# Kernel optimization log

Hardware: AMD Instinct MI355X
Metric: run time of the kernel (lower is better)

## Reference

```python
import jax, jax.numpy as jnp
import numpy as np

B, D, H, C = 8192, 2048, 4096, 64
HALF = D // 2
BLOCKS = 2


def setup_inputs() -> dict:
    key = jax.random.key(0)
    ks = jax.random.split(key, 8)
    z = jax.random.normal(ks[0], (B, D), jnp.float32)
    condition = jax.random.normal(ks[1], (B, C), jnp.float32)
    # alternating masks: block 0 identity=odd indices, transform=even; block 1 flipped
    even = jnp.arange(0, D, 2, dtype=jnp.int32)
    odd = jnp.arange(1, D, 2, dtype=jnp.int32)
    idx_id = jnp.stack([odd, even])   # [BLOCKS, HALF]
    idx_tr = jnp.stack([even, odd])   # [BLOCKS, HALF]
    def init_w(k, shape, fan_in):
        return jax.random.normal(k, shape, jnp.float32) * np.float32(1.0 / np.sqrt(fan_in))
    W1 = init_w(ks[2], (BLOCKS, HALF + C, H), HALF + C)
    b1 = jnp.zeros((BLOCKS, H), jnp.float32)
    W2 = init_w(ks[3], (BLOCKS, H, H), H)
    b2 = jnp.zeros((BLOCKS, H), jnp.float32)
    W3 = init_w(ks[4], (BLOCKS, H, 2 * HALF), H) * np.float32(0.01)  # keep exp(S) tame
    b3 = jnp.zeros((BLOCKS, 2 * HALF), jnp.float32)
    return {"z": z, "condition": condition, "idx_id": idx_id, "idx_tr": idx_tr,
            "W1": W1, "b1": b1, "W2": W2, "b2": b2, "W3": W3, "b3": b3}


def reference(z, condition, idx_id, idx_tr, W1, b1, W2, b2, W3, b3):
    # F_zx of the affine coupling layer (scale_tanh=False, clamp_scale=None)
    x = z
    log_det = jnp.zeros((z.shape[0], 1), z.dtype)
    for i in range(BLOCKS):
        # gather identity channels, condition on external vector
        h = jnp.concatenate([x[:, idx_id[i]], condition], axis=-1)  # [B, HALF+C]
        h = jax.nn.relu(h @ W1[i] + b1[i])
        h = jax.nn.relu(h @ W2[i] + b2[i])
        out = (h @ W3[i] + b3[i]).reshape(x.shape[0], HALF, 2)
        S = out[..., 0]  # scale logits
        T = out[..., 1]  # translation
        # scatter-update transformed channels
        x = x.at[:, idx_tr[i]].set(x[:, idx_tr[i]] * jnp.exp(S) + T)
        log_det = log_det + jnp.sum(S, axis=1, keepdims=True)
    return x, log_det
```

## Files before the change

### kernel.cpp

```cpp
#include <hip/hip_runtime.h>
#include <hip/hip_bf16.h>

#define B_    8192
#define D_    2048
#define H_    4096
#define C_    64
#define HALF_ 1024
#define KIN_  1088

typedef __attribute__((ext_vector_type(8))) short bf16x8;
typedef __attribute__((ext_vector_type(4))) float f32x4;

__device__ __forceinline__ unsigned short f2bf(float f) {
  __hip_bfloat16 h = __float2bfloat16(f);
  return *reinterpret_cast<unsigned short*>(&h);
}

__device__ __forceinline__ void gload16(const void* g, void* s) {
  __builtin_amdgcn_global_load_lds((const __attribute__((address_space(1))) void*)g,
                                   (__attribute__((address_space(3))) void*)s,
                                   16, 0, 0);
}

__global__ void convT(const float* __restrict__ W, unsigned short* __restrict__ Wt,
                      int K, int N) {
  __shared__ float tile[32][33];
  int tx = threadIdx.x & 31, ty = threadIdx.x >> 5;
  int n0 = blockIdx.x * 32, k0 = blockIdx.y * 32;
#pragma unroll
  for (int i = 0; i < 4; ++i)
    tile[ty + i * 8][tx] = W[(size_t)(k0 + ty + i * 8) * N + n0 + tx];
  __syncthreads();
#pragma unroll
  for (int i = 0; i < 4; ++i)
    Wt[(size_t)(n0 + ty + i * 8) * K + k0 + tx] = f2bf(tile[tx][ty + i * 8]);
}

__global__ void build_act(const float* __restrict__ xsrc, const float* __restrict__ cond,
                          int par, unsigned short* __restrict__ A0) {
  int row = blockIdx.y;
  int col = blockIdx.x * 256 + threadIdx.x;
  if (col >= KIN_) return;
  float v;
  if (col < HALF_) {
    float2 p = ((const float2*)xsrc)[(size_t)row * (D_ / 2) + col];
    v = par ? p.y : p.x;
  } else {
    v = cond[(size_t)row * C_ + (col - HALF_)];
  }
  A0[(size_t)row * KIN_ + col] = f2bf(v);
}

template <int MODE>
__global__ __launch_bounds__(512, 2)
void gemm8p(const unsigned short* __restrict__ A,
            const unsigned short* __restrict__ Bt,
            const float* __restrict__ bias,
            unsigned short* __restrict__ Cout,
            const float* __restrict__ xold, float* __restrict__ xnew,
            float* __restrict__ part, int par,
            int M, int N, int K) {
  __shared__ unsigned short lds[65536];
  char* ldsb = (char*)lds;
  const int tid = threadIdx.x;
  const int w = tid >> 6, lane = tid & 63;
  const int fr = lane & 15, fq = lane >> 4;
  const int wr = w >> 2, wc = w & 3;

  const int nbx = N >> 8;
  const int nwg = (int)gridDim.x;
  const int cpx = nwg >> 3;
  const int bid = (int)blockIdx.x;
  const int swz = (bid & 7) * cpx + (bid >> 3);
  const int by = swz / nbx, bx = swz - by * nbx;
  const int m0 = by << 8, n0 = bx << 8;

  const int chunkp = (((fr & 1) << 2) | fq) ^ (fr >> 1);
  const int A0 = (wr * 64 + (fr >> 1)) * 128 + chunkp * 16;
  const int B0 = 16384 + (wc * 32 + (fr >> 1)) * 128 + chunkp * 16;

  int rS[2], kcolS[2];
#pragma unroll
  for (int s = 0; s < 2; ++s) {
    int q = s * 512 + w * 64 + lane;
    int p = q >> 3, cph = q & 7;
    int clg = cph ^ (p & 7);
    rS[s] = 2 * p + (clg >> 2);
    kcolS[s] = (clg & 3) * 8;
  }
  const unsigned short* sA0 = A + (size_t)(m0 + rS[0]) * K + kcolS[0];
  const unsigned short* sA1 = A + (size_t)(m0 + rS[1]) * K + kcolS[1];
  const unsigned short* sB0 = Bt + (size_t)(n0 + rS[0]) * K + kcolS[0];
  const unsigned short* sB1 = Bt + (size_t)(n0 + rS[1]) * K + kcolS[1];
  const int dst0 = w * 1024 + lane * 16;

#define STAGE_ALL(OFF) do {                                                  \
    gload16(sA0, ldsb + (OFF) + dst0);                                       \
    gload16(sA1, ldsb + (OFF) + 8192 + dst0);                                \
    gload16(sB0, ldsb + (OFF) + 16384 + dst0);                               \
    gload16(sB1, ldsb + (OFF) + 24576 + dst0);                               \
    sA0 += 32; sA1 += 32; sB0 += 32; sB1 += 32;                              \
  } while (0)

#define RDFRAGS(AV, BV, OFF)                                                 \
    _Pragma("unroll") for (int n = 0; n < 4; ++n)                            \
      BV[n] = *(const bf16x8*)(ldsb + (OFF) + B0 + n * 1024);                \
    _Pragma("unroll") for (int m = 0; m < 8; ++m)                            \
      AV[m] = *(const bf16x8*)(ldsb + (OFF) + A0 + m * 1024);

#define MFMA32(AV, BV)                                                       \
    __builtin_amdgcn_s_setprio(1);                                           \
    _Pragma("unroll") for (int m = 0; m < 8; ++m)                            \
      _Pragma("unroll") for (int n = 0; n < 4; ++n)                          \
        acc[m][n] = __builtin_amdgcn_mfma_f32_16x16x32_bf16(                 \
            AV[m], BV[n], acc[m][n], 0, 0, 0);                               \
    __builtin_amdgcn_s_setprio(0);

#define WIN(STG, VM, RD, AVr, BVr, AVm, BVm)                                 \
  {                                                                          \
    if (STG) STAGE_ALL(stg);                                                 \
    if (VM == 1) asm volatile("s_waitcnt vmcnt(4)" ::: "memory");            \
    if (VM == 2) asm volatile("s_waitcnt vmcnt(0)" ::: "memory");            \
    __builtin_amdgcn_sched_barrier(0);                                       \
    __builtin_amdgcn_s_barrier();                                            \
    if (RD) { RDFRAGS(AVr, BVr, nxt) }                                       \
    MFMA32(AVm, BVm)                                                         \
    int _t = cur; cur = nxt; nxt = stg; stg = _t;                            \
  }

  f32x4 acc[8][4];
  f32x4 z4 = {0.f, 0.f, 0.f, 0.f};
#pragma unroll
  for (int m = 0; m < 8; ++m)
#pragma unroll
    for (int n = 0; n < 4; ++n) acc[m][n] = z4;

  const int NT = K >> 5;

  bf16x8 av0[8], bv0[4], av1[8], bv1[4];

  STAGE_ALL(0);
  STAGE_ALL(32768);
  asm volatile("s_waitcnt vmcnt(4)" ::: "memory");
  __builtin_amdgcn_sched_barrier(0);
  __builtin_amdgcn_s_barrier();
  RDFRAGS(av0, bv0, 0)
  int cur = 0, nxt = 32768, stg = 65536;

  for (int P = 0; P < (NT - 2) / 2; ++P) {
    WIN(1, 1, 1, av1, bv1, av0, bv0)
    WIN(1, 1, 1, av0, bv0, av1, bv1)
  }
  WIN(0, 2, 1, av1, bv1, av0, bv0)
  WIN(0, 0, 0, av1, bv1, av1, bv1)
  __builtin_amdgcn_s_barrier();
#undef WIN
#undef MFMA32
#undef RDFRAGS
#undef STAGE_ALL

  if (MODE == 0) {
#pragma unroll
    for (int m = 0; m < 8; ++m)
#pragma unroll
      for (int n = 0; n < 4; ++n) {
        int gcol = n0 + wc * 64 + n * 16 + fr;
        float bb = bias[gcol];
#pragma unroll
        for (int r = 0; r < 4; ++r) {
          float v = fmaxf(acc[m][n][r] + bb, 0.f);
          int lrow = m * 16 + fq * 4 + r;
          *(unsigned short*)(ldsb + w * 16384 + lrow * 128 + ((n ^ fq) * 32) + fr * 2) = f2bf(v);
        }
      }
    asm volatile("s_waitcnt lgkmcnt(0)" ::: "memory");
    __builtin_amdgcn_sched_barrier(0);
    unsigned short* Cb = Cout + (size_t)(m0 + wr * 128) * N + n0 + wc * 64;
    const int sub = lane & 7;
#pragma unroll
    for (int i = 0; i < 16; ++i) {
      int lrow = i * 8 + (lane >> 3);
      int phys = (sub >> 1) ^ ((lrow >> 2) & 3);
      bf16x8 val = *(const bf16x8*)(ldsb + w * 16384 + lrow * 128 + phys * 32 + (sub & 1) * 16);
      *(bf16x8*)(Cb + (size_t)lrow * N + sub * 8) = val;
    }
  } else {
#pragma unroll
    for (int m = 0; m < 8; ++m) {
      float srow[4] = {0.f, 0.f, 0.f, 0.f};
#pragma unroll
      for (int n = 0; n < 4; ++n) {
        int gcol = n0 + wc * 64 + n * 16 + fr;
        float bb = bias[gcol];
#pragma unroll
        for (int r = 0; r < 4; ++r) {
          float v = acc[m][n][r] + bb;
          float vp = __shfl_xor(v, 1);
          if (!(fr & 1)) {
            int grow = m0 + wr * 128 + m * 16 + fq * 4 + r;
            size_t idx = (size_t)grow * N + gcol + par;
            xnew[idx] = xold[idx] * expf(v) + vp;
            srow[r] += v;
          }
        }
      }
#pragma unroll
      for (int r = 0; r < 4; ++r) {
        float s = srow[r];
        s += __shfl_xor(s, 2);
        s += __shfl_xor(s, 4);
        s += __shfl_xor(s, 8);
        if (fr == 0) {
          int grow = m0 + wr * 128 + m * 16 + fq * 4 + r;
          part[(size_t)grow * 32 + bx * 4 + wc] = s;
        }
      }
    }
  }
}

__global__ void reduce_logdet(const float* __restrict__ P, float* __restrict__ logdet, int add) {
  int row = blockIdx.x * 256 + threadIdx.x;
  float s = 0.f;
#pragma unroll
  for (int g = 0; g < 32; ++g) s += P[(size_t)row * 32 + g];
  logdet[row] = add ? (logdet[row] + s) : s;
}

extern "C" void kernel_launch(void* const* d_in, const int* in_sizes, int n_in,
                              void* d_out, int out_size, void* d_ws, size_t ws_size,
                              hipStream_t stream) {
  const float* z    = (const float*)d_in[0];
  const float* cond = (const float*)d_in[1];
  const float* W1   = (const float*)d_in[4];
  const float* b1   = (const float*)d_in[5];
  const float* W2   = (const float*)d_in[6];
  const float* b2   = (const float*)d_in[7];
  const float* W3   = (const float*)d_in[8];
  const float* b3   = (const float*)d_in[9];

  float* xout   = (float*)d_out;
  float* logdet = xout + (size_t)B_ * D_;

  char* ws = (char*)d_ws;
  unsigned short* Wt = (unsigned short*)ws;
  unsigned short* H1 = (unsigned short*)(ws + 33554432);
  unsigned short* H2 = (unsigned short*)(ws + 33554432 + 67108864);
  float* Pp = (float*)H1;
  unsigned short* A0 = H2;

  for (int blk = 0; blk < 2; ++blk) {
    const float* W1b = W1 + (size_t)blk * KIN_ * H_;
    const float* W2b = W2 + (size_t)blk * H_ * H_;
    const float* W3b = W3 + (size_t)blk * H_ * D_;
    const float* b1b = b1 + (size_t)blk * H_;
    const float* b2b = b2 + (size_t)blk * H_;
    const float* b3b = b3 + (size_t)blk * D_;
    const float* xsrc = blk ? xout : z;

    convT<<<dim3(H_ / 32, KIN_ / 32), 256, 0, stream>>>(W1b, Wt, KIN_, H_);
    build_act<<<dim3(5, B_), 256, 0, stream>>>(xsrc, cond, 1 - blk, A0);
    gemm8p<0><<<dim3((H_ / 256) * (B_ / 256)), 512, 0, stream>>>(
        A0, Wt, b1b, H1, nullptr, nullptr, nullptr, 0, B_, H_, KIN_);

    convT<<<dim3(H_ / 32, H_ / 32), 256, 0, stream>>>(W2b, Wt, H_, H_);
    gemm8p<0><<<dim3((H_ / 256) * (B_ / 256)), 512, 0, stream>>>(
        H1, Wt, b2b, H2, nullptr, nullptr, nullptr, 0, B_, H_, H_);

    convT<<<dim3(D_ / 32, H_ / 32), 256, 0, stream>>>(W3b, Wt, H_, D_);
    gemm8p<1><<<dim3((D_ / 256) * (B_ / 256)), 512, 0, stream>>>(
        H2, Wt, b3b, nullptr, z, xout, Pp, blk, B_, D_, H_);

    reduce_logdet<<<dim3(B_ / 256), 256, 0, stream>>>(Pp, logdet, blk);
  }
}
```

Baseline: 1.022 ms.

## Shrink GEMM tile to 256x128 with single-buffered fragments for higher occupancy

Reduces the GEMM macro-tile from 256x256 to 256x128, with 8 waves in a 4x2 layout each computing 64x64. This halves the accumulator registers and cuts LDS to a 3-stage 72KB ring, so launch bounds can request 4 blocks per CU. The register double-buffered fragment pipeline becomes a simpler loop that reads fragments, issues the next stage's loads, then runs the MFMAs. The aim is more occupancy and more blocks in flight, at the cost of lower arithmetic intensity per tile and more global traffic for the A operand.

```diff
diff --git a/kernel.cpp b/kernel.cpp
--- a/kernel.cpp
+++ b/kernel.cpp
@@ -52,31 +52,31 @@
 }
 
 template <int MODE>
-__global__ __launch_bounds__(512, 2)
-void gemm8p(const unsigned short* __restrict__ A,
-            const unsigned short* __restrict__ Bt,
-            const float* __restrict__ bias,
-            unsigned short* __restrict__ Cout,
-            const float* __restrict__ xold, float* __restrict__ xnew,
-            float* __restrict__ part, int par,
-            int M, int N, int K) {
-  __shared__ unsigned short lds[65536];
+__global__ __launch_bounds__(512, 4)
+void gemmk(const unsigned short* __restrict__ A,
+           const unsigned short* __restrict__ Bt,
+           const float* __restrict__ bias,
+           unsigned short* __restrict__ Cout,
+           const float* __restrict__ xold, float* __restrict__ xnew,
+           float* __restrict__ part, int par,
+           int M, int N, int K) {
+  __shared__ unsigned short lds[36864];
   char* ldsb = (char*)lds;
   const int tid = threadIdx.x;
   const int w = tid >> 6, lane = tid & 63;
   const int fr = lane & 15, fq = lane >> 4;
-  const int wr = w >> 2, wc = w & 3;
-
-  const int nbx = N >> 8;
+  const int wr = w >> 1, wc = w & 1;
+
+  const int nbx = N >> 7;
   const int nwg = (int)gridDim.x;
   const int cpx = nwg >> 3;
   const int bid = (int)blockIdx.x;
   const int swz = (bid & 7) * cpx + (bid >> 3);
   const int by = swz / nbx, bx = swz - by * nbx;
-  const int m0 = by << 8, n0 = bx << 8;
+  const int m0 = by << 8, n0 = bx << 7;
 
   const int chunkp = (((fr & 1) << 2) | fq) ^ (fr >> 1);
-  const int A0 = (wr * 64 + (fr >> 1)) * 128 + chunkp * 16;
+  const int A0 = (wr * 32 + (fr >> 1)) * 128 + chunkp * 16;
   const int B0 = 16384 + (wc * 32 + (fr >> 1)) * 128 + chunkp * 16;
 
   int rS[2], kcolS[2];
@@ -91,77 +91,65 @@
   const unsigned short* sA0 = A + (size_t)(m0 + rS[0]) * K + kcolS[0];
   const unsigned short* sA1 = A + (size_t)(m0 + rS[1]) * K + kcolS[1];
   const unsigned short* sB0 = Bt + (size_t)(n0 + rS[0]) * K + kcolS[0];
-  const unsigned short* sB1 = Bt + (size_t)(n0 + rS[1]) * K + kcolS[1];
   const int dst0 = w * 1024 + lane * 16;
 
 #define STAGE_ALL(OFF) do {                                                  \
     gload16(sA0, ldsb + (OFF) + dst0);                                       \
     gload16(sA1, ldsb + (OFF) + 8192 + dst0);                                \
     gload16(sB0, ldsb + (OFF) + 16384 + dst0);                               \
-    gload16(sB1, ldsb + (OFF) + 24576 + dst0);                               \
-    sA0 += 32; sA1 += 32; sB0 += 32; sB1 += 32;                              \
+    sA0 += 32; sA1 += 32; sB0 += 32;                                         \
   } while (0)
 
-#define RDFRAGS(AV, BV, OFF)                                                 \
+#define WIN(STG, VM)                                                         \
+  {                                                                          \
+    __builtin_amdgcn_s_barrier();                                            \
+    __builtin_amdgcn_sched_barrier(0);                                       \
+    bf16x8 av[4], bv[4];                                                     \
     _Pragma("unroll") for (int n = 0; n < 4; ++n)                            \
-      BV[n] = *(const bf16x8*)(ldsb + (OFF) + B0 + n * 1024);                \
-    _Pragma("unroll") for (int m = 0; m < 8; ++m)                            \
-      AV[m] = *(const bf16x8*)(ldsb + (OFF) + A0 + m * 1024);
-
-#define MFMA32(AV, BV)                                                       \
+      bv[n] = *(const bf16x8*)(ldsb + cur + B0 + n * 1024);                  \
+    _Pragma("unroll") for (int m = 0; m < 4; ++m)                            \
+      av[m] = *(const bf16x8*)(ldsb + cur + A0 + m * 1024);                  \
+    if (STG) STAGE_ALL(stg);                                                 \
     __builtin_amdgcn_s_setprio(1);                                           \
-    _Pragma("unroll") for (int m = 0; m < 8; ++m)                            \
+    _Pragma("unroll") for (int m = 0; m < 4; ++m)                            \
       _Pragma("unroll") for (int n = 0; n < 4; ++n)                          \
         acc[m][n] = __builtin_amdgcn_mfma_f32_16x16x32_bf16(                 \
-            AV[m], BV[n], acc[m][n], 0, 0, 0);                               \
-    __builtin_amdgcn_s_setprio(0);
-
-#define WIN(STG, VM, RD, AVr, BVr, AVm, BVm)                                 \
-  {                                                                          \
-    if (STG) STAGE_ALL(stg);                                                 \
-    if (VM == 1) asm volatile("s_waitcnt vmcnt(4)" ::: "memory");            \
+            av[m], bv[n], acc[m][n], 0, 0, 0);                               \
+    __builtin_amdgcn_s_setprio(0);                                           \
+    if (VM == 1) asm volatile("s_waitcnt vmcnt(3)" ::: "memory");            \
     if (VM == 2) asm volatile("s_waitcnt vmcnt(0)" ::: "memory");            \
     __builtin_amdgcn_sched_barrier(0);                                       \
-    __builtin_amdgcn_s_barrier();                                            \
-    if (RD) { RDFRAGS(AVr, BVr, nxt) }                                       \
-    MFMA32(AVm, BVm)                                                         \
-    int _t = cur; cur = nxt; nxt = stg; stg = _t;                            \
-  }
-
-  f32x4 acc[8][4];
+    cur = (cur == 49152) ? 0 : cur + 24576;                                  \
+    stg = (stg == 49152) ? 0 : stg + 24576;                                  \
+  }
+
+  f32x4 acc[4][4];
   f32x4 z4 = {0.f, 0.f, 0.f, 0.f};
 #pragma unroll
-  for (int m = 0; m < 8; ++m)
+  for (int m = 0; m < 4; ++m)
 #pragma unroll
     for (int n = 0; n < 4; ++n) acc[m][n] = z4;
 
   const int NT = K >> 5;
 
-  bf16x8 av0[8], bv0[4], av1[8], bv1[4];
-
   STAGE_ALL(0);
-  STAGE_ALL(32768);
-  asm volatile("s_waitcnt vmcnt(4)" ::: "memory");
+  STAGE_ALL(24576);
+  asm volatile("s_waitcnt vmcnt(3)" ::: "memory");
   __builtin_amdgcn_sched_barrier(0);
-  __builtin_amdgcn_s_barrier();
-  RDFRAGS(av0, bv0, 0)
-  int cur = 0, nxt = 32768, stg = 65536;
-
-  for (int P = 0; P < (NT - 2) / 2; ++P) {
-    WIN(1, 1, 1, av1, bv1, av0, bv0)
-    WIN(1, 1, 1, av0, bv0, av1, bv1)
-  }
-  WIN(0, 2, 1, av1, bv1, av0, bv0)
-  WIN(0, 0, 0, av1, bv1, av1, bv1)
-  __builtin_amdgcn_s_barrier();
+  int cur = 0, stg = 49152;
+
+  for (int T = 0; T < NT - 2; ++T) {
+    WIN(1, 1)
+  }
+  WIN(0, 2)
+  WIN(0, 0)
 #undef WIN
-#undef MFMA32
-#undef RDFRAGS
 #undef STAGE_ALL
 
   if (MODE == 0) {
-#pragma unroll
-    for (int m = 0; m < 8; ++m)
+    __builtin_amdgcn_s_barrier();
+#pragma unroll
+    for (int m = 0; m < 4; ++m)
 #pragma unroll
       for (int n = 0; n < 4; ++n) {
         int gcol = n0 + wc * 64 + n * 16 + fr;
@@ -170,23 +158,23 @@
         for (int r = 0; r < 4; ++r) {
           float v = fmaxf(acc[m][n][r] + bb, 0.f);
           int lrow = m * 16 + fq * 4 + r;
-          *(unsigned short*)(ldsb + w * 16384 + lrow * 128 + ((n ^ fq) * 32) + fr * 2) = f2bf(v);
+          *(unsigned short*)(ldsb + w * 8192 + lrow * 128 + ((n ^ fq) * 32) + fr * 2) = f2bf(v);
         }
       }
     asm volatile("s_waitcnt lgkmcnt(0)" ::: "memory");
     __builtin_amdgcn_sched_barrier(0);
-    unsigned short* Cb = Cout + (size_t)(m0 + wr * 128) * N + n0 + wc * 64;
+    unsigned short* Cb = Cout + (size_t)(m0 + wr * 64) * N + n0 + wc * 64;
     const int sub = lane & 7;
 #pragma unroll
-    for (int i = 0; i < 16; ++i) {
+    for (int i = 0; i < 8; ++i) {
       int lrow = i * 8 + (lane >> 3);
       int phys = (sub >> 1) ^ ((lrow >> 2) & 3);
-      bf16x8 val = *(const bf16x8*)(ldsb + w * 16384 + lrow * 128 + phys * 32 + (sub & 1) * 16);
+      bf16x8 val = *(const bf16x8*)(ldsb + w * 8192 + lrow * 128 + phys * 32 + (sub & 1) * 16);
       *(bf16x8*)(Cb + (size_t)lrow * N + sub * 8) = val;
     }
   } else {
 #pragma unroll
-    for (int m = 0; m < 8; ++m) {
+    for (int m = 0; m < 4; ++m) {
       float srow[4] = {0.f, 0.f, 0.f, 0.f};
 #pragma unroll
       for (int n = 0; n < 4; ++n) {
@@ -197,7 +185,7 @@
           float v = acc[m][n][r] + bb;
           float vp = __shfl_xor(v, 1);
           if (!(fr & 1)) {
-            int grow = m0 + wr * 128 + m * 16 + fq * 4 + r;
+            int grow = m0 + wr * 64 + m * 16 + fq * 4 + r;
             size_t idx = (size_t)grow * N + gcol + par;
             xnew[idx] = xold[idx] * expf(v) + vp;
             srow[r] += v;
@@ -211,8 +199,8 @@
         s += __shfl_xor(s, 4);
         s += __shfl_xor(s, 8);
         if (fr == 0) {
-          int grow = m0 + wr * 128 + m * 16 + fq * 4 + r;
-          part[(size_t)grow * 32 + bx * 4 + wc] = s;
+          int grow = m0 + wr * 64 + m * 16 + fq * 4 + r;
+          part[(size_t)grow * 32 + bx * 2 + wc] = s;
         }
       }
     }
@@ -260,15 +248,15 @@
 
     convT<<<dim3(H_ / 32, KIN_ / 32), 256, 0, stream>>>(W1b, Wt, KIN_, H_);
     build_act<<<dim3(5, B_), 256, 0, stream>>>(xsrc, cond, 1 - blk, A0);
-    gemm8p<0><<<dim3((H_ / 256) * (B_ / 256)), 512, 0, stream>>>(
+    gemmk<0><<<dim3((B_ / 256) * (H_ / 128)), 512, 0, stream>>>(
         A0, Wt, b1b, H1, nullptr, nullptr, nullptr, 0, B_, H_, KIN_);
 
     convT<<<dim3(H_ / 32, H_ / 32), 256, 0, stream>>>(W2b, Wt, H_, H_);
-    gemm8p<0><<<dim3((H_ / 256) * (B_ / 256)), 512, 0, stream>>>(
+    gemmk<0><<<dim3((B_ / 256) * (H_ / 128)), 512, 0, stream>>>(
         H1, Wt, b2b, H2, nullptr, nullptr, nullptr, 0, B_, H_, H_);
 
     convT<<<dim3(D_ / 32, H_ / 32), 256, 0, stream>>>(W3b, Wt, H_, D_);
-    gemm8p<1><<<dim3((D_ / 256) * (B_ / 256)), 512, 0, stream>>>(
+    gemmk<1><<<dim3((B_ / 256) * (D_ / 128)), 512, 0, stream>>>(
         H2, Wt, b3b, nullptr, z, xout, Pp, blk, B_, D_, H_);
 
     reduce_logdet<<<dim3(B_ / 256), 256, 0, stream>>>(Pp, logdet, blk);
```

Result: slower. 1.149 ms (+12.4%).
